# Optimization experiments

Hardware: AMD Instinct MI355X
Metric: run time of the kernel (lower is better)

## Reference

```python
import jax, jax.numpy as jnp
import numpy as np

H = 32        # query heads
KV = 8        # kv heads (GQA)
D = 128       # head_dim
HID = 4096    # hidden_size
T = 2048      # tokens (single causal sequence)
THETA = 10000.0


def setup_inputs() -> dict:
    key = jax.random.key(0)
    k1, k2, k3 = jax.random.split(key, 3)
    return {
        "positions": jnp.arange(T, dtype=jnp.int32),
        "hidden_states": jax.random.normal(k1, (T, HID), dtype=jnp.float32),
        "w_qkv": jax.random.normal(k2, ((H + 2 * KV) * D, HID), dtype=jnp.float32) * 0.02,
        "w_o": jax.random.normal(k3, (HID, H * D), dtype=jnp.float32) * 0.02,
    }


def _rope_neox(x, cos, sin):
    # x: [T, h, D]; cos/sin: [T, D/2]
    half = x.shape[-1] // 2
    x1, x2 = x[..., :half], x[..., half:]
    c, s = cos[:, None, :], sin[:, None, :]
    return jnp.concatenate([x1 * c - x2 * s, x2 * c + x1 * s], axis=-1)


def reference(positions, hidden_states, w_qkv, w_o):
    t = hidden_states.shape[0]
    qkv = hidden_states @ w_qkv.T                      # [T, (H+2KV)*D]
    q, k, v = jnp.split(qkv, [H * D, H * D + KV * D], axis=-1)
    q = q.reshape(t, H, D)
    k = k.reshape(t, KV, D)
    v = v.reshape(t, KV, D)

    # neox-style RoPE over full head_dim
    half = D // 2
    inv_freq = 1.0 / (THETA ** (jnp.arange(0, D, 2, dtype=jnp.float32) / D))  # [D/2]
    freqs = positions.astype(jnp.float32)[:, None] * inv_freq                 # [T, D/2]
    cos, sin = jnp.cos(freqs), jnp.sin(freqs)
    q = _rope_neox(q, cos, sin)
    k = _rope_neox(k, cos, sin)

    # GQA: expand kv heads to match query heads
    rep = H // KV
    k = jnp.repeat(k, rep, axis=1)                     # [T, H, D]
    v = jnp.repeat(v, rep, axis=1)

    scale = D ** -0.5
    scores = jnp.einsum('thd,shd->hts', q, k) * scale  # [H, T, T]
    causal = positions[:, None] >= positions[None, :]  # [T, T]
    neg = jnp.finfo(scores.dtype).min
    scores = jnp.where(causal[None], scores, neg)
    attn = jax.nn.softmax(scores, axis=-1)
    out = jnp.einsum('hts,shd->thd', attn, v).reshape(t, H * D)
    return out @ w_o.T                                 # [T, HID]
```

## Files before the change

kernel.cpp:

```cpp
#include <hip/hip_runtime.h>
#include <hip/hip_bf16.h>
#include <cstdint>

typedef __bf16 bf16;
typedef __bf16 bf16x8 __attribute__((ext_vector_type(8)));
typedef float f32x4 __attribute__((ext_vector_type(4)));

#define DEV __device__ __forceinline__

DEV f32x4 mfma16(bf16x8 a, bf16x8 b, f32x4 c) {
  return __builtin_amdgcn_mfma_f32_16x16x32_bf16(a, b, c, 0, 0, 0);
}

DEV void gl2lds16(const void* g, void* l) {
  __builtin_amdgcn_global_load_lds((__attribute__((address_space(1))) void*)g,
                                   (__attribute__((address_space(3))) void*)l,
                                   16, 0, 0);
}

__global__ void cvt_f32_bf16(const float* __restrict__ s, bf16* __restrict__ d, int n) {
  int i = (blockIdx.x * 256 + threadIdx.x) * 8;
  if (i >= n) return;
  f32x4 a = *(const f32x4*)(s + i);
  f32x4 b = *(const f32x4*)(s + i + 4);
  bf16x8 o;
#pragma unroll
  for (int e = 0; e < 4; ++e) { o[e] = (bf16)a[e]; o[e + 4] = (bf16)b[e]; }
  *(bf16x8*)(d + i) = o;
}

template <typename OutT>
__global__ __launch_bounds__(256) void gemm_bt(const bf16* __restrict__ A,
                                               const bf16* __restrict__ B,
                                               OutT* __restrict__ C,
                                               int M, int N, int K) {
  __shared__ bf16 As[128 * 32];
  __shared__ bf16 Bs[128 * 32];
  const int tid = threadIdx.x;
  const int lane = tid & 63, w = tid >> 6;
  const int wm = w & 1, wn = w >> 1;
  const int quad = lane >> 4, r = lane & 15;
  const long mBase = (long)blockIdx.y * 128, nBase = (long)blockIdx.x * 128;
  f32x4 acc[4][4];
#pragma unroll
  for (int i = 0; i < 4; ++i)
#pragma unroll
    for (int j = 0; j < 4; ++j) acc[i][j] = f32x4{0.f, 0.f, 0.f, 0.f};

  for (int k0 = 0; k0 < K; k0 += 32) {
    __syncthreads();
#pragma unroll
    for (int j = 0; j < 2; ++j) {
      const int c = w * 128 + j * 64 + lane;
      const int row = c >> 2, kc = c & 3;
      gl2lds16(A + (mBase + row) * (long)K + k0 + kc * 8,
               (char*)As + (w * 128 + j * 64) * 16);
      gl2lds16(B + (nBase + row) * (long)K + k0 + kc * 8,
               (char*)Bs + (w * 128 + j * 64) * 16);
    }
    __syncthreads();
    bf16x8 af[4], bfr[4];
#pragma unroll
    for (int i = 0; i < 4; ++i) {
      af[i]  = *(const bf16x8*)(&As[(wm * 64 + i * 16 + r) * 32 + quad * 8]);
      bfr[i] = *(const bf16x8*)(&Bs[(wn * 64 + i * 16 + r) * 32 + quad * 8]);
    }
#pragma unroll
    for (int mi = 0; mi < 4; ++mi)
#pragma unroll
      for (int ni = 0; ni < 4; ++ni)
        acc[mi][ni] = mfma16(af[mi], bfr[ni], acc[mi][ni]);
  }
#pragma unroll
  for (int mi = 0; mi < 4; ++mi)
#pragma unroll
    for (int ni = 0; ni < 4; ++ni)
#pragma unroll
      for (int rg = 0; rg < 4; ++rg) {
        long row = mBase + wm * 64 + mi * 16 + quad * 4 + rg;
        long col = nBase + wn * 64 + ni * 16 + r;
        C[row * N + col] = (OutT)acc[mi][ni][rg];
      }
}

__global__ void rope_kernel(bf16* __restrict__ qkv, const int* __restrict__ pos) {
  int idx = blockIdx.x * 256 + threadIdx.x;
  int d = idx & 63;
  int rest = idx >> 6;
  int head = rest % 40;
  int t = rest / 40;
  bf16* p = qkv + (long)t * 6144 + head * 128;
  float x1 = (float)p[d], x2 = (float)p[d + 64];
  float inv_freq = __builtin_expf(-(float)d * (9.210340371976184f / 64.0f));
  float fr = (float)pos[t] * inv_freq;
  float c = __builtin_cosf(fr), s = __builtin_sinf(fr);
  p[d]      = (bf16)(x1 * c - x2 * s);
  p[d + 64] = (bf16)(x2 * c + x1 * s);
}

__global__ __launch_bounds__(256, 3) void attn_kernel(const bf16* __restrict__ qkv,
                                                      bf16* __restrict__ out) {
  constexpr int LDV = 72, LDP = 72;
  constexpr float SCL2 = 0.08838834764831845f * 1.4426950408889634f;
  __shared__ bf16 Ks[64 * 128];
  __shared__ bf16 Vt[128 * LDV];
  __shared__ bf16 Ps[64 * LDP];
  const int tid = threadIdx.x;
  const int lane = tid & 63, w = tid >> 6;
  const int quad = lane >> 4, r = lane & 15;
  const int pr = blockIdx.x, h = blockIdx.y;
  const int kvh = h >> 2;

  for (int which = 0; which < 2; ++which) {
    const int qt = which ? (31 - pr) : pr;
    const int rowq = qt * 64 + w * 16;

    bf16x8 qf[4];
#pragma unroll
    for (int ks = 0; ks < 4; ++ks)
      qf[ks] = *(const bf16x8*)(qkv + (long)(rowq + r) * 6144 + h * 128 + ks * 32 + quad * 8);

    f32x4 of[8];
#pragma unroll
    for (int di = 0; di < 8; ++di) of[di] = f32x4{0.f, 0.f, 0.f, 0.f};
    float mrun[4], lrun[4];
#pragma unroll
    for (int rg = 0; rg < 4; ++rg) { mrun[rg] = -__builtin_inff(); lrun[rg] = 0.f; }

    const int ntiles = qt + 1;
    for (int kt = 0; kt < ntiles; ++kt) {
      const int kvbase = kt * 64;
      __syncthreads();

#pragma unroll
      for (int ii = 0; ii < 4; ++ii) {
        const int c = ii * 256 + tid;
        const int row = c >> 4;
        const int dcg = (c & 15) ^ (row & 15);
        gl2lds16(qkv + (long)(kvbase + row) * 6144 + 4096 + kvh * 128 + dcg * 8,
                 (char*)Ks + (ii * 256 + w * 64) * 16);
      }
#pragma unroll
      for (int ii = 0; ii < 4; ++ii) {
        const int c = ii * 256 + tid;
        const int j = c >> 4, dc = c & 15;
        bf16x8 v = *(const bf16x8*)(qkv + (long)(kvbase + j) * 6144 + 5120 + kvh * 128 + dc * 8);
        const int pc = (((j >> 3) ^ (dc & 7)) << 3) + (j & 7);
#pragma unroll
        for (int e = 0; e < 8; ++e) Vt[(dc * 8 + e) * LDV + pc] = v[e];
      }
      __syncthreads();

      f32x4 sacc[4];
#pragma unroll
      for (int ni = 0; ni < 4; ++ni) sacc[ni] = f32x4{0.f, 0.f, 0.f, 0.f};
#pragma unroll
      for (int ks = 0; ks < 4; ++ks) {
        bf16x8 kf[4];
#pragma unroll
        for (int ni = 0; ni < 4; ++ni)
          kf[ni] = *(const bf16x8*)(&Ks[(ni * 16 + r) * 128 + (((ks * 4 + quad) ^ r) << 3)]);
#pragma unroll
        for (int ni = 0; ni < 4; ++ni) sacc[ni] = mfma16(qf[ks], kf[ni], sacc[ni]);
      }

      float mt[4];
#pragma unroll
      for (int rg = 0; rg < 4; ++rg) mt[rg] = -1e30f;
      const int rq = rowq + quad * 4;
#pragma unroll
      for (int ni = 0; ni < 4; ++ni) {
        const int ck = kvbase + ni * 16 + r;
#pragma unroll
        for (int rg = 0; rg < 4; ++rg) {
          float sv = sacc[ni][rg];
          sv = (ck > rq + rg) ? -1e30f : sv;
          sacc[ni][rg] = sv;
          mt[rg] = fmaxf(mt[rg], sv);
        }
      }
#pragma unroll
      for (int rg = 0; rg < 4; ++rg) {
        float v = mt[rg];
        v = fmaxf(v, __shfl_xor(v, 1));
        v = fmaxf(v, __shfl_xor(v, 2));
        v = fmaxf(v, __shfl_xor(v, 4));
        v = fmaxf(v, __shfl_xor(v, 8));
        mt[rg] = v;
      }
      float alpha[4], rsum[4];
#pragma unroll
      for (int rg = 0; rg < 4; ++rg) {
        const float mnew = fmaxf(mrun[rg], mt[rg]);
        alpha[rg] = __builtin_exp2f((mrun[rg] - mnew) * SCL2);
        mrun[rg] = mnew;
        rsum[rg] = 0.f;
      }
#pragma unroll
      for (int ni = 0; ni < 4; ++ni)
#pragma unroll
        for (int rg = 0; rg < 4; ++rg) {
          const float pv = __builtin_exp2f((sacc[ni][rg] - mrun[rg]) * SCL2);
          rsum[rg] += pv;
          Ps[(w * 16 + quad * 4 + rg) * LDP + ni * 16 + r] = (bf16)pv;
        }
#pragma unroll
      for (int rg = 0; rg < 4; ++rg) {
        float v = rsum[rg];
        v += __shfl_xor(v, 1);
        v += __shfl_xor(v, 2);
        v += __shfl_xor(v, 4);
        v += __shfl_xor(v, 8);
        lrun[rg] = lrun[rg] * alpha[rg] + v;
      }
#pragma unroll
      for (int di = 0; di < 8; ++di)
#pragma unroll
        for (int rg = 0; rg < 4; ++rg) of[di][rg] *= alpha[rg];

#pragma unroll
      for (int js = 0; js < 2; ++js) {
        const bf16x8 pf = *(const bf16x8*)(&Ps[(w * 16 + r) * LDP + js * 32 + quad * 8]);
#pragma unroll
        for (int di = 0; di < 8; ++di) {
          const int vrow = di * 16 + r;
          const int vcol = (((js * 4 + quad) ^ ((vrow >> 3) & 7)) << 3);
          const bf16x8 vf = *(const bf16x8*)(&Vt[vrow * LDV + vcol]);
          of[di] = mfma16(pf, vf, of[di]);
        }
      }
    }

#pragma unroll
    for (int rg = 0; rg < 4; ++rg) {
      const float inv = 1.f / lrun[rg];
      const long t = rowq + quad * 4 + rg;
#pragma unroll
      for (int di = 0; di < 8; ++di)
        out[t * 4096 + h * 128 + di * 16 + r] = (bf16)(of[di][rg] * inv);
    }
  }
}

extern "C" void kernel_launch(void* const* d_in, const int* in_sizes, int n_in,
                              void* d_out, int out_size, void* d_ws, size_t ws_size,
                              hipStream_t stream) {
  const int* positions = (const int*)d_in[0];
  const float* hidden = (const float*)d_in[1];
  const float* w_qkv = (const float*)d_in[2];
  const float* w_o = (const float*)d_in[3];
  float* out = (float*)d_out;

  char* ws = (char*)d_ws;
  bf16* hid_b  = (bf16*)(ws);
  bf16* wqkv_b = (bf16*)(ws + 16777216);
  bf16* wo_b   = (bf16*)(ws + 67108864);
  bf16* qkv    = (bf16*)(ws + 100663296);
  bf16* attn   = (bf16*)(ws + 125829120);

  cvt_f32_bf16<<<8388608 / 2048, 256, 0, stream>>>(hidden, hid_b, 8388608);
  cvt_f32_bf16<<<25165824 / 2048, 256, 0, stream>>>(w_qkv, wqkv_b, 25165824);
  cvt_f32_bf16<<<16777216 / 2048, 256, 0, stream>>>(w_o, wo_b, 16777216);
  gemm_bt<bf16><<<dim3(48, 16), 256, 0, stream>>>(hid_b, wqkv_b, qkv, 2048, 6144, 4096);
  rope_kernel<<<5242880 / 256, 256, 0, stream>>>(qkv, positions);
  attn_kernel<<<dim3(16, 32), 256, 0, stream>>>(qkv, attn);
  gemm_bt<float><<<dim3(32, 16), 256, 0, stream>>>(attn, wo_b, out, 2048, 4096, 4096);
}
```

Measured before the change: 584.9 us.

## Fuse conversions, swizzle GEMM LDS, vectorize RoPE, prefetch KV in attention

Merges the three f32-to-bf16 conversion launches into one kernel. Applies an XOR swizzle to the GEMM LDS tiles to reduce bank conflicts. Vectorizes RoPE to eight elements per thread. In attention, the next K/V tile is prefetched into registers while the current tile is computed, causal masking is skipped on tiles below the diagonal, and the occupancy hint drops from 3 to 2 waves. The extra prefetch registers may lower occupancy.

```diff
diff --git a/kernel.cpp b/kernel.cpp
--- a/kernel.cpp
+++ b/kernel.cpp
@@ -18,15 +18,24 @@
                                    16, 0, 0);
 }
 
-__global__ void cvt_f32_bf16(const float* __restrict__ s, bf16* __restrict__ d, int n) {
-  int i = (blockIdx.x * 256 + threadIdx.x) * 8;
-  if (i >= n) return;
-  f32x4 a = *(const f32x4*)(s + i);
-  f32x4 b = *(const f32x4*)(s + i + 4);
+DEV void cvt8(const float* __restrict__ s, bf16* __restrict__ d) {
+  f32x4 a = *(const f32x4*)(s);
+  f32x4 b = *(const f32x4*)(s + 4);
   bf16x8 o;
 #pragma unroll
   for (int e = 0; e < 4; ++e) { o[e] = (bf16)a[e]; o[e + 4] = (bf16)b[e]; }
-  *(bf16x8*)(d + i) = o;
+  *(bf16x8*)(d) = o;
+}
+
+__global__ void cvt3(const float* __restrict__ s0, bf16* __restrict__ d0, int n0,
+                     const float* __restrict__ s1, bf16* __restrict__ d1, int n1,
+                     const float* __restrict__ s2, bf16* __restrict__ d2) {
+  long i = ((long)blockIdx.x * 256 + threadIdx.x) * 8;
+  if (i < n0) { cvt8(s0 + i, d0 + i); return; }
+  i -= n0;
+  if (i < n1) { cvt8(s1 + i, d1 + i); return; }
+  i -= n1;
+  cvt8(s2 + i, d2 + i);
 }
 
 template <typename OutT>
@@ -53,17 +62,18 @@
     for (int j = 0; j < 2; ++j) {
       const int c = w * 128 + j * 64 + lane;
       const int row = c >> 2, kc = c & 3;
-      gl2lds16(A + (mBase + row) * (long)K + k0 + kc * 8,
+      const int kcx = kc ^ (row & 3);
+      gl2lds16(A + (mBase + row) * (long)K + k0 + kcx * 8,
                (char*)As + (w * 128 + j * 64) * 16);
-      gl2lds16(B + (nBase + row) * (long)K + k0 + kc * 8,
+      gl2lds16(B + (nBase + row) * (long)K + k0 + kcx * 8,
                (char*)Bs + (w * 128 + j * 64) * 16);
     }
     __syncthreads();
     bf16x8 af[4], bfr[4];
 #pragma unroll
     for (int i = 0; i < 4; ++i) {
-      af[i]  = *(const bf16x8*)(&As[(wm * 64 + i * 16 + r) * 32 + quad * 8]);
-      bfr[i] = *(const bf16x8*)(&Bs[(wn * 64 + i * 16 + r) * 32 + quad * 8]);
+      af[i]  = *(const bf16x8*)(&As[(wm * 64 + i * 16 + r) * 32 + ((quad ^ (r & 3)) << 3)]);
+      bfr[i] = *(const bf16x8*)(&Bs[(wn * 64 + i * 16 + r) * 32 + ((quad ^ (r & 3)) << 3)]);
     }
 #pragma unroll
     for (int mi = 0; mi < 4; ++mi)
@@ -85,20 +95,30 @@
 
 __global__ void rope_kernel(bf16* __restrict__ qkv, const int* __restrict__ pos) {
   int idx = blockIdx.x * 256 + threadIdx.x;
-  int d = idx & 63;
-  int rest = idx >> 6;
+  int g = idx & 7;
+  int rest = idx >> 3;
   int head = rest % 40;
   int t = rest / 40;
-  bf16* p = qkv + (long)t * 6144 + head * 128;
-  float x1 = (float)p[d], x2 = (float)p[d + 64];
-  float inv_freq = __builtin_expf(-(float)d * (9.210340371976184f / 64.0f));
-  float fr = (float)pos[t] * inv_freq;
-  float c = __builtin_cosf(fr), s = __builtin_sinf(fr);
-  p[d]      = (bf16)(x1 * c - x2 * s);
-  p[d + 64] = (bf16)(x2 * c + x1 * s);
-}
-
-__global__ __launch_bounds__(256, 3) void attn_kernel(const bf16* __restrict__ qkv,
+  bf16* p = qkv + (long)t * 6144 + head * 128 + g * 8;
+  bf16x8 a = *(const bf16x8*)(p);
+  bf16x8 b = *(const bf16x8*)(p + 64);
+  const float pf = (float)pos[t];
+  bf16x8 oa, ob;
+#pragma unroll
+  for (int e = 0; e < 8; ++e) {
+    const int d = g * 8 + e;
+    const float invf = __builtin_expf(-(float)d * (9.210340371976184f / 64.0f));
+    const float fr = pf * invf;
+    const float c = __builtin_cosf(fr), s = __builtin_sinf(fr);
+    const float x1 = (float)a[e], x2 = (float)b[e];
+    oa[e] = (bf16)(x1 * c - x2 * s);
+    ob[e] = (bf16)(x2 * c + x1 * s);
+  }
+  *(bf16x8*)(p) = oa;
+  *(bf16x8*)(p + 64) = ob;
+}
+
+__global__ __launch_bounds__(256, 2) void attn_kernel(const bf16* __restrict__ qkv,
                                                       bf16* __restrict__ out) {
   constexpr int LDV = 72, LDP = 72;
   constexpr float SCL2 = 0.08838834764831845f * 1.4426950408889634f;
@@ -111,6 +131,15 @@
   const int pr = blockIdx.x, h = blockIdx.y;
   const int kvh = h >> 2;
 
+  bf16x8 kreg[4], vreg[4];
+  int srow[4], sdc[4];
+#pragma unroll
+  for (int ii = 0; ii < 4; ++ii) {
+    const int c = ii * 256 + tid;
+    srow[ii] = c >> 4;
+    sdc[ii] = c & 15;
+  }
+
   for (int which = 0; which < 2; ++which) {
     const int qt = which ? (31 - pr) : pr;
     const int rowq = qt * 64 + w * 16;
@@ -128,28 +157,34 @@
     for (int rg = 0; rg < 4; ++rg) { mrun[rg] = -__builtin_inff(); lrun[rg] = 0.f; }
 
     const int ntiles = qt + 1;
+#pragma unroll
+    for (int ii = 0; ii < 4; ++ii) {
+      const long rb = (long)srow[ii] * 6144 + kvh * 128;
+      kreg[ii] = *(const bf16x8*)(qkv + rb + 4096 + sdc[ii] * 8);
+      vreg[ii] = *(const bf16x8*)(qkv + rb + 5120 + sdc[ii] * 8);
+    }
+
     for (int kt = 0; kt < ntiles; ++kt) {
       const int kvbase = kt * 64;
       __syncthreads();
-
 #pragma unroll
       for (int ii = 0; ii < 4; ++ii) {
-        const int c = ii * 256 + tid;
-        const int row = c >> 4;
-        const int dcg = (c & 15) ^ (row & 15);
-        gl2lds16(qkv + (long)(kvbase + row) * 6144 + 4096 + kvh * 128 + dcg * 8,
-                 (char*)Ks + (ii * 256 + w * 64) * 16);
-      }
-#pragma unroll
-      for (int ii = 0; ii < 4; ++ii) {
-        const int c = ii * 256 + tid;
-        const int j = c >> 4, dc = c & 15;
-        bf16x8 v = *(const bf16x8*)(qkv + (long)(kvbase + j) * 6144 + 5120 + kvh * 128 + dc * 8);
-        const int pc = (((j >> 3) ^ (dc & 7)) << 3) + (j & 7);
-#pragma unroll
-        for (int e = 0; e < 8; ++e) Vt[(dc * 8 + e) * LDV + pc] = v[e];
+        const int row = srow[ii], dc = sdc[ii];
+        *(bf16x8*)(&Ks[row * 128 + ((dc ^ (row & 15)) << 3)]) = kreg[ii];
+        const int pc = (((row >> 3) ^ (dc & 7)) << 3) + (row & 7);
+#pragma unroll
+        for (int e = 0; e < 8; ++e) Vt[(dc * 8 + e) * LDV + pc] = vreg[ii][e];
       }
       __syncthreads();
+      {
+        const int kvn = (kt + 1 < ntiles) ? (kt + 1) * 64 : kt * 64;
+#pragma unroll
+        for (int ii = 0; ii < 4; ++ii) {
+          const long rb = (long)(kvn + srow[ii]) * 6144 + kvh * 128;
+          kreg[ii] = *(const bf16x8*)(qkv + rb + 4096 + sdc[ii] * 8);
+          vreg[ii] = *(const bf16x8*)(qkv + rb + 5120 + sdc[ii] * 8);
+        }
+      }
 
       f32x4 sacc[4];
 #pragma unroll
@@ -167,17 +202,24 @@
       float mt[4];
 #pragma unroll
       for (int rg = 0; rg < 4; ++rg) mt[rg] = -1e30f;
-      const int rq = rowq + quad * 4;
-#pragma unroll
-      for (int ni = 0; ni < 4; ++ni) {
-        const int ck = kvbase + ni * 16 + r;
-#pragma unroll
-        for (int rg = 0; rg < 4; ++rg) {
-          float sv = sacc[ni][rg];
-          sv = (ck > rq + rg) ? -1e30f : sv;
-          sacc[ni][rg] = sv;
-          mt[rg] = fmaxf(mt[rg], sv);
+      if (kt == qt) {
+        const int rq = rowq + quad * 4;
+#pragma unroll
+        for (int ni = 0; ni < 4; ++ni) {
+          const int ck = kvbase + ni * 16 + r;
+#pragma unroll
+          for (int rg = 0; rg < 4; ++rg) {
+            float sv = sacc[ni][rg];
+            sv = (ck > rq + rg) ? -1e30f : sv;
+            sacc[ni][rg] = sv;
+            mt[rg] = fmaxf(mt[rg], sv);
+          }
         }
+      } else {
+#pragma unroll
+        for (int ni = 0; ni < 4; ++ni)
+#pragma unroll
+          for (int rg = 0; rg < 4; ++rg) mt[rg] = fmaxf(mt[rg], sacc[ni][rg]);
       }
 #pragma unroll
       for (int rg = 0; rg < 4; ++rg) {
@@ -258,11 +300,11 @@
   bf16* qkv    = (bf16*)(ws + 100663296);
   bf16* attn   = (bf16*)(ws + 125829120);
 
-  cvt_f32_bf16<<<8388608 / 2048, 256, 0, stream>>>(hidden, hid_b, 8388608);
-  cvt_f32_bf16<<<25165824 / 2048, 256, 0, stream>>>(w_qkv, wqkv_b, 25165824);
-  cvt_f32_bf16<<<16777216 / 2048, 256, 0, stream>>>(w_o, wo_b, 16777216);
+  cvt3<<<24576, 256, 0, stream>>>(hidden, hid_b, 8388608,
+                                  w_qkv, wqkv_b, 25165824,
+                                  w_o, wo_b);
   gemm_bt<bf16><<<dim3(48, 16), 256, 0, stream>>>(hid_b, wqkv_b, qkv, 2048, 6144, 4096);
-  rope_kernel<<<5242880 / 256, 256, 0, stream>>>(qkv, positions);
+  rope_kernel<<<2560, 256, 0, stream>>>(qkv, positions);
   attn_kernel<<<dim3(16, 32), 256, 0, stream>>>(qkv, attn);
   gemm_bt<float><<<dim3(32, 16), 256, 0, stream>>>(attn, wo_b, out, 2048, 4096, 4096);
 }
```

New measurement: 573.4 us. Within noise of the previous version (-2.0%).
